# Kernel tuning notes

Hardware: AMD Instinct MI355X
Metric: run time of the kernel (lower is better)

## Reference

```python
import jax, jax.numpy as jnp
import numpy as np
from jax import lax

B, T = 4, 2048
IN_CH, SKIP_CH, OUT_CH, K = 256, 128, 128, 5
N_MAMBA, D_STATE, D_CONV, EXPAND = 2, 16, 4, 2
D_INNER = EXPAND * OUT_CH
DT_RANK = (OUT_CH + 15) // 16  # ceil(d_model/16) = 8
L = 2 * T
EPS = 1e-5


def setup_inputs() -> dict:
    key = jax.random.key(0)
    ks = jax.random.split(key, 16)
    def rn(k, shape, s=0.02):
        return jax.random.normal(k, shape, jnp.float32) * s
    A_init = jnp.broadcast_to(jnp.arange(1, D_STATE + 1, dtype=jnp.float32),
                              (N_MAMBA, 2, D_INNER, D_STATE))
    return {
        'x': rn(ks[0], (B, IN_CH, T), 1.0),
        'skip': rn(ks[1], (B, SKIP_CH, L), 1.0),
        'up_w': rn(ks[2], (IN_CH, IN_CH, K)),       # torch ConvTranspose1d weight (in,out,k)
        'up_b': jnp.zeros((IN_CH,), jnp.float32),
        'fus_w': rn(ks[3], (OUT_CH, IN_CH + SKIP_CH)),  # 1x1 conv
        'fus_b': jnp.zeros((OUT_CH,), jnp.float32),
        'gn_w': jnp.ones((OUT_CH,), jnp.float32),
        'gn_b': jnp.zeros((OUT_CH,), jnp.float32),
        'prelu_a': jnp.array(0.25, jnp.float32),
        'ln_w': jnp.ones((N_MAMBA, OUT_CH), jnp.float32),
        'ln_b': jnp.zeros((N_MAMBA, OUT_CH), jnp.float32),
        'in_w': rn(ks[4], (N_MAMBA, 2, 2 * D_INNER, OUT_CH)),
        'conv_w': rn(ks[5], (N_MAMBA, 2, D_INNER, D_CONV), 0.1),
        'conv_b': jnp.zeros((N_MAMBA, 2, D_INNER), jnp.float32),
        'xproj_w': rn(ks[6], (N_MAMBA, 2, DT_RANK + 2 * D_STATE, D_INNER)),
        'dtproj_w': rn(ks[7], (N_MAMBA, 2, D_INNER, DT_RANK), 0.1),
        'dtproj_b': rn(ks[8], (N_MAMBA, 2, D_INNER), 0.1),
        'A_log': jnp.log(A_init),
        'Dp': jnp.ones((N_MAMBA, 2, D_INNER), jnp.float32),
        'out_w': rn(ks[9], (N_MAMBA, 2, OUT_CH, D_INNER)),
    }


def _mamba_branch(xn, cw, cb, iw, xw, dw, db, Alog, Dp, ow):
    # xn: [B, L, d_model] -> [B, L, d_model]; standard Mamba selective scan.
    xz = jnp.einsum('bld,ed->ble', xn, iw)            # [B,L,2*D_INNER]
    xi, z = jnp.split(xz, 2, axis=-1)
    # causal depthwise conv over time
    xc = lax.conv_general_dilated(xi.transpose(0, 2, 1), cw[:, None, :], (1,),
                                  [(D_CONV - 1, 0)], feature_group_count=D_INNER,
                                  dimension_numbers=('NCH', 'OIH', 'NCH'))
    xi = jax.nn.silu(xc + cb[None, :, None]).transpose(0, 2, 1)  # [B,L,D_INNER]
    dbl = jnp.einsum('bld,ed->ble', xi, xw)           # [B,L,DT_RANK+2N]
    dt = jax.nn.softplus(jnp.einsum('blr,dr->bld', dbl[..., :DT_RANK], dw) + db)
    Bc = dbl[..., DT_RANK:DT_RANK + D_STATE]          # [B,L,N]
    Cc = dbl[..., DT_RANK + D_STATE:]                 # [B,L,N]
    A = -jnp.exp(Alog)                                # [D_INNER,N]
    dA = jnp.exp(dt[..., None] * A)                   # [B,L,D_INNER,N]
    dBx = dt[..., None] * Bc[:, :, None, :] * xi[..., None]
    def comb(c1, c2):
        a1, b1 = c1
        a2, b2 = c2
        return a1 * a2, a2 * b1 + b2
    _, h = lax.associative_scan(comb, (dA, dBx), axis=1)  # h_t = dA_t h_{t-1} + dBx_t
    y = jnp.einsum('bldn,bln->bld', h, Cc) + Dp * xi
    return jnp.einsum('ble,de->bld', y * jax.nn.silu(z), ow)


def _forward(x, skip, up_w, up_b, fus_w, fus_b, gn_w, gn_b, prelu_a, ln_w, ln_b,
             in_w, conv_w, conv_b, xproj_w, dtproj_w, dtproj_b, A_log, Dp, out_w):
    p = K // 2
    # ConvTranspose1d(stride=2, padding=p, output_padding=1) == lhs-dilated conv with flipped kernel
    wt = jnp.flip(up_w, -1).transpose(1, 0, 2)        # (out,in,k)
    u = lax.conv_general_dilated(x, wt, (1,), [(K - 1 - p, K - 1 - p + 1)],
                                 lhs_dilation=(2,),
                                 dimension_numbers=('NCH', 'OIH', 'NCH'))
    u = u + up_b[None, :, None]
    u = u[..., :skip.shape[-1]]
    h = jnp.concatenate([u, skip], axis=1)            # [B, in+skip, L]
    h = jnp.einsum('bct,oc->bot', h, fus_w) + fus_b[None, :, None]
    # GroupNorm(1, C): normalize over (C,T) per sample
    mu = h.mean(axis=(1, 2), keepdims=True)
    var = h.var(axis=(1, 2), keepdims=True)
    h = (h - mu) / jnp.sqrt(var + EPS) * gn_w[None, :, None] + gn_b[None, :, None]
    h = jnp.where(h >= 0, h, prelu_a * h)             # PReLU (single param)
    h = h.transpose(0, 2, 1)                          # [B, L, C]
    for i in range(N_MAMBA):
        # BiMambaBlock: pre-LN, forward + time-reversed Mamba, residual sum
        mu2 = h.mean(-1, keepdims=True)
        v2 = h.var(-1, keepdims=True)
        xn = (h - mu2) / jnp.sqrt(v2 + EPS) * ln_w[i] + ln_b[i]
        f = _mamba_branch(xn, conv_w[i, 0], conv_b[i, 0], in_w[i, 0], xproj_w[i, 0],
                          dtproj_w[i, 0], dtproj_b[i, 0], A_log[i, 0], Dp[i, 0], out_w[i, 0])
        b = _mamba_branch(jnp.flip(xn, 1), conv_w[i, 1], conv_b[i, 1], in_w[i, 1], xproj_w[i, 1],
                          dtproj_w[i, 1], dtproj_b[i, 1], A_log[i, 1], Dp[i, 1], out_w[i, 1])
        h = h + f + jnp.flip(b, 1)
    return h.transpose(0, 2, 1)                       # [B, C_out, L]


def reference(x, skip, up_w, up_b, fus_w, fus_b, gn_w, gn_b, prelu_a, ln_w, ln_b,
              in_w, conv_w, conv_b, xproj_w, dtproj_w, dtproj_b, A_log, Dp, out_w):
    return _forward(x, skip, up_w, up_b, fus_w, fus_b, gn_w, gn_b, prelu_a, ln_w, ln_b,
                    in_w, conv_w, conv_b, xproj_w, dtproj_w, dtproj_b, A_log, Dp, out_w)
```

## Files before the change

### kernel.cpp

```cpp
#include <hip/hip_runtime.h>
#include <hip/hip_bf16.h>

#define Bsz 4
#define Tt 2048
#define Ll 4096
#define NC 256
#define CH 16

typedef short bf16x8 __attribute__((ext_vector_type(8)));
typedef float f32x4 __attribute__((ext_vector_type(4)));
typedef float f32x2 __attribute__((ext_vector_type(2)));

static __device__ __forceinline__ f32x2 pk_fma(f32x2 a, f32x2 b, f32x2 c){
  f32x2 d;
  asm("v_pk_fma_f32 %0, %1, %2, %3" : "=v"(d) : "v"(a), "v"(b), "v"(c));
  return d;
}
static __device__ __forceinline__ f32x2 pk_mul(f32x2 a, f32x2 b){
  f32x2 d;
  asm("v_pk_mul_f32 %0, %1, %2" : "=v"(d) : "v"(a), "v"(b));
  return d;
}

static __device__ __forceinline__ float bs2f(unsigned short u){
  union{float f; unsigned int i;} v; v.i = ((unsigned int)u)<<16; return v.f;
}
static __device__ __forceinline__ unsigned short f2bs(float f){
  union{float f; unsigned int i;} v; v.f = f;
  unsigned int r = (v.i + 0x7fffu + ((v.i>>16)&1u)) >> 16;
  return (unsigned short)r;
}

__global__ void k_cvt(const float* __restrict__ src, unsigned short* __restrict__ dst, int n){
  int i = blockIdx.x*256 + threadIdx.x;
  if (i < n) dst[i] = f2bs(src[i]);
}

__global__ void k_prepx(const float* __restrict__ xw, unsigned short* __restrict__ wxb){
  int row = blockIdx.x, br = blockIdx.y, col = threadIdx.x;
  float v = (row < 40) ? xw[((size_t)br*40 + row)*256 + col] : 0.f;
  wxb[((size_t)br*64 + row)*256 + col] = f2bs(v);
}

__global__ void k_compose(const float* __restrict__ up_w, const float* __restrict__ fus_w,
                          const float* __restrict__ fus_b, const float* __restrict__ up_b,
                          unsigned short* __restrict__ WEb, unsigned short* __restrict__ WOb,
                          unsigned short* __restrict__ FWSb, float* __restrict__ BIAS2){
  int i = blockIdx.x;
  int o = threadIdx.x;
  float a0=0.f,a1=0.f,a2=0.f,a3=0.f,a4=0.f;
  for (int c=0;c<256;c++){
    float f = fus_w[o*384+c];
    const float* w = up_w + ((size_t)i*256+c)*5;
    a0 += f*w[0]; a1 += f*w[1]; a2 += f*w[2];
    a3 += f*w[3]; a4 += f*w[4];
  }
  WEb[(size_t)o*768 +       i] = f2bs(a4);
  WEb[(size_t)o*768 + 256 + i] = f2bs(a2);
  WEb[(size_t)o*768 + 512 + i] = f2bs(a0);
  WOb[(size_t)o*512 +       i] = f2bs(a3);
  WOb[(size_t)o*512 + 256 + i] = f2bs(a1);
  if (i<128) FWSb[o*128 + i] = f2bs(fus_w[o*384+256+i]);
  if (i==0){
    float bb = fus_b[o];
    for (int c=0;c<256;c++) bb += fus_w[o*384+c]*up_b[c];
    BIAS2[o]=bb;
  }
}

__global__ __launch_bounds__(256) void k_tx(const float* __restrict__ x, unsigned short* __restrict__ XT){
  __shared__ float tile[64][65];
  int b=blockIdx.z, t0=blockIdx.x*64, i0=blockIdx.y*64;
  int tid=threadIdx.x;
  for (int it=0;it<16;it++){
    int idx=it*256+tid; int ii=idx>>6, tt=idx&63;
    tile[ii][tt] = x[((size_t)b*256+i0+ii)*Tt + t0+tt];
  }
  __syncthreads();
  for (int it=0;it<16;it++){
    int idx=it*256+tid; int tt=idx>>6, ii=idx&63;
    XT[((size_t)b*2050 + t0+tt+1)*256 + i0+ii] = f2bs(tile[ii][tt]);
  }
}

__global__ void k_zero(unsigned short* __restrict__ XT){
  int tid=threadIdx.x;
  for (int b=0;b<Bsz;b++){
    XT[((size_t)b*2050)*256 + tid] = 0;
    XT[((size_t)b*2050+2049)*256 + tid] = 0;
  }
}

__global__ __launch_bounds__(256) void k_ts(const float* __restrict__ skip, unsigned short* __restrict__ SKT){
  __shared__ float tile[64][65];
  int b=blockIdx.z, l0=blockIdx.x*64, s0=blockIdx.y*64;
  int tid=threadIdx.x;
  for (int it=0;it<16;it++){
    int idx=it*256+tid; int ss=idx>>6, ll=idx&63;
    tile[ss][ll] = skip[((size_t)b*128+s0+ss)*Ll + l0+ll];
  }
  __syncthreads();
  for (int it=0;it<16;it++){
    int idx=it*256+tid; int ll=idx>>6, ss=idx&63;
    SKT[((size_t)b*Ll + l0+ll)*128 + s0+ss] = f2bs(tile[ss][ll]);
  }
}

__global__ __launch_bounds__(256) void k_up(const unsigned short* __restrict__ XT,
                     const unsigned short* __restrict__ SKT,
                     const unsigned short* __restrict__ WEb, const unsigned short* __restrict__ WOb,
                     const unsigned short* __restrict__ FWSb, const float* __restrict__ B2,
                     float* __restrict__ h0, float* __restrict__ gst){
  __shared__ unsigned short XL[66*264];
  __shared__ unsigned short Wb[128*72];
  __shared__ float red0[256], red1[256];
  int bt = blockIdx.x, par = blockIdx.y, b = blockIdx.z;
  int t0 = bt*64;
  int tid = threadIdx.x;
  int wave = tid>>6, lane = tid&63;
  int wm = wave>>1, wn = wave&1;
  int quad = lane>>4, l16 = lane&15;

  for (int idx=tid; idx<66*32; idx+=256){
    int row = idx>>5, c8 = idx&31;
// ... 52 lines not shown
      *(uint4*)&Wb[row*72 + c8*8] = *(const uint4*)&FWSb[(size_t)row*128 + kc*64 + c8*8];
    }
    __syncthreads();
    #pragma unroll
    for (int ks=0; ks<64; ks+=32){
      bf16x8 af[2], bf[4];
      #pragma unroll
      for (int mt=0;mt<2;mt++)
        af[mt] = *(bf16x8*)&XL[(wm*32+mt*16+l16)*136 + kc*64 + ks + quad*8];
      #pragma unroll
      for (int nt=0;nt<4;nt++)
        bf[nt] = *(bf16x8*)&Wb[(wn*64+nt*16+l16)*72 + ks + quad*8];
      #pragma unroll
      for (int mt=0;mt<2;mt++)
        #pragma unroll
        for (int nt=0;nt<4;nt++)
          acc[mt][nt] = __builtin_amdgcn_mfma_f32_16x16x32_bf16(af[mt], bf[nt], acc[mt][nt], 0,0,0);
    }
  }

  float s1=0.f, s2=0.f;
  #pragma unroll
  for (int mt=0;mt<2;mt++)
    #pragma unroll
    for (int nt=0;nt<4;nt++)
      #pragma unroll
      for (int r=0;r<4;r++){
        int m = wm*32 + mt*16 + quad*4 + r;
        int lrow = 2*(t0+m) + par;
        int col = wn*64 + nt*16 + l16;
        float v = acc[mt][nt][r] + B2[col];
        h0[((size_t)b*Ll + lrow)*128 + col] = v;
        s1 += v; s2 += v*v;
      }
  red0[tid]=s1; red1[tid]=s2;
  __syncthreads();
  for (int st=128; st>0; st>>=1){
    if (tid<st){ red0[tid]+=red0[tid+st]; red1[tid]+=red1[tid+st]; }
    __syncthreads();
  }
  if (tid==0){ atomicAdd(&gst[b*2], red0[0]); atomicAdd(&gst[b*2+1], red1[0]); }
}

__global__ void k_gnfin(float* gst){
  int b = threadIdx.x;
  if (b < Bsz){
    float n = (float)Ll*128.f;
    float mu = gst[b*2]/n;
    float var = gst[b*2+1]/n - mu*mu;
    gst[8+b]=mu; gst[12+b]=rsqrtf(var+1e-5f);
  }
}

__global__ __launch_bounds__(256) void k_gnln(const float* __restrict__ h0, const float* __restrict__ gn_w,
                      const float* __restrict__ gn_b, const float* __restrict__ pa,
                      const float* __restrict__ gst, const float* __restrict__ lnw,
                      const float* __restrict__ lnb, float* __restrict__ hres,
                      unsigned short* __restrict__ xn){
  int row = blockIdx.x*4 + (threadIdx.x>>6);
  int lane = threadIdx.x & 63;
  int b = row >> 12;
  float mu_g = gst[8+b], inv_g = gst[12+b];
  float a = pa[0];
  const float* hp = h0 + (size_t)row*128;
  float u0 = (hp[lane]   -mu_g)*inv_g*gn_w[lane]    + gn_b[lane];
  float u1 = (hp[lane+64]-mu_g)*inv_g*gn_w[lane+64] + gn_b[lane+64];
  float v0 = u0>=0.f ? u0 : a*u0;
  float v1 = u1>=0.f ? u1 : a*u1;
  float* rp = hres + (size_t)row*128;
  rp[lane] = v0; rp[lane+64] = v1;
  float s = v0+v1, q = v0*v0+v1*v1;
  #pragma unroll
  for (int off=32; off>0; off>>=1){
    s += __shfl_xor(s, off, 64);
    q += __shfl_xor(q, off, 64);
  }
  float mu = s*(1.f/128.f);
  float rs = rsqrtf(q*(1.f/128.f)-mu*mu + 1e-5f);
  unsigned short* xp = xn + (size_t)row*128;
  xp[lane]    = f2bs((v0-mu)*rs*lnw[lane]    + lnb[lane]);
  xp[lane+64] = f2bs((v1-mu)*rs*lnw[lane+64] + lnb[lane+64]);
}

__global__ __launch_bounds__(256) void k_ln(const float* __restrict__ hres, const float* __restrict__ lnw,
                     const float* __restrict__ lnb, unsigned short* __restrict__ xn){
  int row = blockIdx.x*4 + (threadIdx.x>>6);
  int lane = threadIdx.x & 63;
  const float* hp = hres + (size_t)row*128;
  float v0 = hp[lane], v1 = hp[lane+64];
  float s = v0+v1, q = v0*v0+v1*v1;
  #pragma unroll
  for (int off=32; off>0; off>>=1){
    s += __shfl_xor(s, off, 64);
    q += __shfl_xor(q, off, 64);
  }
  float mu = s*(1.f/128.f);
  float rs = rsqrtf(q*(1.f/128.f)-mu*mu + 1e-5f);
  unsigned short* xp = xn + (size_t)row*128;
  xp[lane]    = f2bs((v0-mu)*rs*lnw[lane]    + lnb[lane]);
  xp[lane+64] = f2bs((v1-mu)*rs*lnw[lane+64] + lnb[lane+64]);
}

__global__ __launch_bounds__(256) void k_gemm_in(const unsigned short* __restrict__ A,
                          const unsigned short* __restrict__ W,
                          unsigned short* __restrict__ C){
  __shared__ unsigned short As[128*72];
  __shared__ unsigned short Bs[128*72];
  int tid = threadIdx.x;
  int row0 = blockIdx.x*128;
  int n0   = blockIdx.y*128;
  int dir  = blockIdx.z;
  const unsigned short* Wp = W + (size_t)dir*512*128;
  unsigned short* Cp = C + (size_t)dir*Bsz*Ll*512;
  int wave = tid>>6, lane = tid&63;
  int wm = wave>>1, wn = wave&1;
  int quad = lane>>4, l16 = lane&15;
  f32x4 acc[4][4];
  #pragma unroll
  for (int i=0;i<4;i++)
    #pragma unroll
    for (int j=0;j<4;j++) acc[i][j] = (f32x4){0.f,0.f,0.f,0.f};

  for (int kb=0; kb<128; kb+=64){
    __syncthreads();
    #pragma unroll
    for (int it=0; it<4; it++){
      int idx = it*256 + tid;
      int row = idx>>3, c8 = idx&7;
      int r = row0 + row;
      int p = r & (Ll-1); int bb = r >> 12;
      int src = (bb<<12) + (dir ? (Ll-1-p) : p);
      *(uint4*)&As[row*72 + c8*8] = *(const uint4*)&A[(size_t)src*128 + kb + c8*8];
      *(uint4*)&Bs[row*72 + c8*8] = *(const uint4*)&Wp[(size_t)(n0+row)*128 + kb + c8*8];
    }
    __syncthreads();
    #pragma unroll
    for (int ks=0; ks<64; ks+=32){
      bf16x8 af[4], bf[4];
      #pragma unroll
      for (int mt=0;mt<4;mt++)
        af[mt] = *(bf16x8*)&As[(wm*64+mt*16+l16)*72 + ks + quad*8];
      #pragma unroll
      for (int nt=0;nt<4;nt++)
        bf[nt] = *(bf16x8*)&Bs[(wn*64+nt*16+l16)*72 + ks + quad*8];
      #pragma unroll
      for (int mt=0;mt<4;mt++)
        #pragma unroll
        for (int nt=0;nt<4;nt++)
          acc[mt][nt] = __builtin_amdgcn_mfma_f32_16x16x32_bf16(af[mt], bf[nt], acc[mt][nt], 0,0,0);
    }
  }
  #pragma unroll
  for (int mt=0;mt<4;mt++)
    #pragma unroll
    for (int nt=0;nt<4;nt++)
      #pragma unroll
      for (int r=0;r<4;r++){
        int row = row0 + wm*64 + mt*16 + quad*4 + r;
        int col = n0 + wn*64 + nt*16 + l16;
        Cp[(size_t)row*512 + col] = f2bs(acc[mt][nt][r]);
      }
}

__global__ __launch_bounds__(256) void k_gemm_out(const unsigned short* __restrict__ Y,
                           const unsigned short* __restrict__ W,
                           float* __restrict__ C){
  __shared__ unsigned short As[64*72];
  __shared__ unsigned short Bs[128*72];
  int tid = threadIdx.x;
  int row0 = blockIdx.x*64;
  int wave = tid>>6, lane = tid&63;
  int wm = wave>>1, wn = wave&1;
  int quad = lane>>4, l16 = lane&15;
  const size_t planeY = (size_t)Bsz*Ll*256;
  f32x4 acc[2][4];
  #pragma unroll
  for (int i=0;i<2;i++)
    #pragma unroll
    for (int j=0;j<4;j++) acc[i][j] = (f32x4){0.f,0.f,0.f,0.f};

  for (int kc=0; kc<8; kc++){
    int dirp = kc>>2;
    int kb = (kc&3)*64;
    const unsigned short* Wp = W + (size_t)dirp*128*256;
    __syncthreads();
    #pragma unroll
    for (int it=0; it<2; it++){
      int idx = it*256 + tid;
      int row = idx>>3, c8 = idx&7;
      int r = row0 + row;
      int p = r & (Ll-1); int bb = r >> 12;
      int srow = dirp ? ((bb<<12) + (Ll-1-p)) : r;
      *(uint4*)&As[row*72 + c8*8] = *(const uint4*)&Y[dirp*planeY + (size_t)srow*256 + kb + c8*8];
    }
    #pragma unroll
    for (int it=0; it<4; it++){
      int idx = it*256 + tid;
      int row = idx>>3, c8 = idx&7;
      *(uint4*)&Bs[row*72 + c8*8] = *(const uint4*)&Wp[(size_t)row*256 + kb + c8*8];
    }
    __syncthreads();
    #pragma unroll
    for (int ks=0; ks<64; ks+=32){
      bf16x8 af[2], bf[4];
      #pragma unroll
      for (int mt=0;mt<2;mt++)
        af[mt] = *(bf16x8*)&As[(wm*32+mt*16+l16)*72 + ks + quad*8];
      #pragma unroll
      for (int nt=0;nt<4;nt++)
        bf[nt] = *(bf16x8*)&Bs[(wn*64+nt*16+l16)*72 + ks + quad*8];
      #pragma unroll
      for (int mt=0;mt<2;mt++)
        #pragma unroll
        for (int nt=0;nt<4;nt++)
          acc[mt][nt] = __builtin_amdgcn_mfma_f32_16x16x32_bf16(af[mt], bf[nt], acc[mt][nt], 0,0,0);
    }
  }
  #pragma unroll
  for (int mt=0;mt<2;mt++)
    #pragma unroll
    for (int nt=0;nt<4;nt++)
      #pragma unroll
      for (int r=0;r<4;r++){
        int row = row0 + wm*32 + mt*16 + quad*4 + r;
        int col = wn*64 + nt*16 + l16;
        C[(size_t)row*128 + col] += acc[mt][nt][r];
      }
}

__global__ __launch_bounds__(256) void k_xproj3(const unsigned short* __restrict__ xz,
                        const unsigned short* __restrict__ wxb,
                        const float* __restrict__ cw, const float* __restrict__ cb,
                        unsigned short* __restrict__ xib, float* __restrict__ dbl){
  __shared__ unsigned short xiS[64*264];
  __shared__ unsigned short Bs[64*72];
  int tid = threadIdx.x;
  int dir = blockIdx.y;
  xz  += (size_t)dir*Bsz*Ll*512;
  wxb += (size_t)dir*64*256;
  cw  += dir*1024;
  cb  += dir*256;
  xib += (size_t)dir*Bsz*Ll*256;
  dbl += (size_t)dir*Bsz*Ll*40;
  size_t row0 = (size_t)blockIdx.x*64;
  int p0 = (int)(row0 & (Ll-1));

  {
    int d = tid;
    float4 w4 = *(const float4*)&cw[d*4];
    float bias = cb[d];
    float w0, w1, w2;
    if (p0 == 0){ w0=0.f; w1=0.f; w2=0.f; }
    else {
      w0 = bs2f(xz[(row0-3)*512 + d]);
      w1 = bs2f(xz[(row0-2)*512 + d]);
      w2 = bs2f(xz[(row0-1)*512 + d]);
    }
    #pragma unroll 4
    for (int rr=0; rr<64; rr++){
      float xv = bs2f(xz[(row0+rr)*512 + d]);
      float acc = bias + w4.x*w0 + w4.y*w1 + w4.z*w2 + w4.w*xv;
      float v = acc*__builtin_amdgcn_rcpf(1.f+__expf(-acc));
      unsigned short us = f2bs(v);
      xiS[rr*264 + d] = us;
      xib[(row0+rr)*256 + d] = us;
      w0=w1; w1=w2; w2=xv;
    }
  }

  int wave = tid>>6, lane = tid&63;
  int quad = lane>>4, l16 = lane&15;
  f32x4 acc[4];
  #pragma unroll
  for (int j=0;j<4;j++) acc[j] = (f32x4){0.f,0.f,0.f,0.f};

  for (int kb=0; kb<256; kb+=64){
    __syncthreads();
    #pragma unroll
    for (int it=0; it<2; it++){
      int idx = it*256 + tid;
      int row = idx>>3, c8 = idx&7;
      *(uint4*)&Bs[row*72 + c8*8] = *(const uint4*)&wxb[(size_t)row*256 + kb + c8*8];
    }
    __syncthreads();
    #pragma unroll
    for (int ks=0; ks<64; ks+=32){
      bf16x8 af = *(bf16x8*)&xiS[(wave*16+l16)*264 + kb + ks + quad*8];
      #pragma unroll
      for (int nt=0;nt<4;nt++){
        bf16x8 bf = *(bf16x8*)&Bs[(nt*16+l16)*72 + ks + quad*8];
        acc[nt] = __builtin_amdgcn_mfma_f32_16x16x32_bf16(af, bf, acc[nt], 0,0,0);
      }
    }
  }
  #pragma unroll
  for (int nt=0;nt<4;nt++)
    #pragma unroll
    for (int r=0;r<4;r++){
      int m = wave*16 + quad*4 + r;
      int col = nt*16 + l16;
      if (col < 40) dbl[(row0+m)*40 + col] = acc[nt][r];
    }
}

#define POWTREE2(e1, pw2) { \
  float _e2 = (e1)*(e1); \
  f32x2 _e2v = (f32x2){_e2,_e2}; \
  pw2[0] = (f32x2){(e1),_e2}; \
  pw2[1] = pk_mul(pw2[0], _e2v); \
  pw2[2] = pk_mul(pw2[1], _e2v); \
  pw2[3] = pk_mul(pw2[2], _e2v); \
  f32x2 _e8v = (f32x2){pw2[3].y, pw2[3].y}; \
  pw2[4] = pk_mul(pw2[0], _e8v); \
  pw2[5] = pk_mul(pw2[1], _e8v); \
  pw2[6] = pk_mul(pw2[2], _e8v); \
  pw2[7] = pk_mul(pw2[3], _e8v); }

__global__ __launch_bounds__(256) void k_scan1(const float* __restrict__ dbl,
                       const unsigned short* __restrict__ xib, const float* __restrict__ Alog,
                       const float* __restrict__ dtw, const float* __restrict__ dtb,
                       float* __restrict__ SD, float* __restrict__ Q){
  __shared__ float dblS[CH*24];
  int b = blockIdx.y, c = blockIdx.x, dir = blockIdx.z;
  int d = threadIdx.x;
  const float* dblP = dbl + (size_t)dir*Bsz*Ll*40;
  const unsigned short* xiP = xib + (size_t)dir*Bsz*Ll*256;
  size_t base = (size_t)b*Ll + (size_t)c*CH;
  if (d < CH*6){
    int p = d/6, j = d - p*6;
    *(float4*)&dblS[p*24 + j*4] = *(const float4*)&dblP[(base+p)*40 + j*4];
  }
  float A[16];
  #pragma unroll
  for (int j=0;j<4;j++){
    float4 a4 = *(const float4*)&Alog[(size_t)dir*4096 + d*16 + j*4];
    A[4*j]=-__expf(a4.x); A[4*j+1]=-__expf(a4.y); A[4*j+2]=-__expf(a4.z); A[4*j+3]=-__expf(a4.w);
  }
  bool chain = true;
  #pragma unroll
  for (int n=1;n<16;n++){
    float expect = A[0]*(float)(n+1);
    if (fabsf(A[n]-expect) > 1e-3f*fabsf(expect)) chain = false;
  }
  f32x2 wv2[4];
  {
    const float* dw = dtw + (size_t)dir*2048 + d*8;
    float4 w0 = *(const float4*)&dw[0];
    float4 w1 = *(const float4*)&dw[4];
    wv2[0]=(f32x2){w0.x,w0.y}; wv2[1]=(f32x2){w0.z,w0.w};
    wv2[2]=(f32x2){w1.x,w1.y}; wv2[3]=(f32x2){w1.z,w1.w};
  }
  float bbt = dtb[dir*256 + d];
  __syncthreads();
  float sdt = 0.f;
  const unsigned short* xip = xiP + base*256 + d;
  size_t sbase = (size_t)dir*Bsz*NC*4096 + ((size_t)(b*NC + c))*4096 + (size_t)d*16;
  if (chain){
    float A0 = A[0];
    bool n1 = fabsf(A0 + 1.f) < 1e-6f;
    f32x2 h2[8];
    #pragma unroll
    for (int i=0;i<8;i++) h2[i] = (f32x2){0.f,0.f};
    #pragma unroll 2
    for (int p=0;p<CH;p++){
      const float* rw = &dblS[p*24];
      f32x4 t0 = *(const f32x4*)&rw[0];
      f32x4 t1 = *(const f32x4*)&rw[4];
      f32x2 dp = pk_mul((f32x2){t0.x,t0.y}, wv2[0]);
      dp = pk_fma((f32x2){t0.z,t0.w}, wv2[1], dp);
      dp = pk_fma((f32x2){t1.x,t1.y}, wv2[2], dp);
      dp = pk_fma((f32x2){t1.z,t1.w}, wv2[3], dp);
      float a0 = bbt + dp.x + dp.y;
      float t = __expf(a0);
      float u = 1.f + t;
      float dtv = (a0>20.f)? a0 : __logf(u);
      float e1 = n1 ? __builtin_amdgcn_rcpf(u) : __expf(dtv*A0);
      float xiv = bs2f(xip[(size_t)p*256]);
      float dx = dtv*xiv;
      sdt += dtv;
      f32x2 pw2[8];
      POWTREE2(e1, pw2);
      f32x2 dxv = (f32x2){dx,dx};
      f32x4 b0 = *(const f32x4*)&rw[8];
      f32x4 b1 = *(const f32x4*)&rw[12];
      f32x4 b2 = *(const f32x4*)&rw[16];
      f32x4 b3 = *(const f32x4*)&rw[20];
      f32x2 bc2[8] = {{b0.x,b0.y},{b0.z,b0.w},{b1.x,b1.y},{b1.z,b1.w},
                      {b2.x,b2.y},{b2.z,b2.w},{b3.x,b3.y},{b3.z,b3.w}};
      #pragma unroll
      for (int i=0;i<8;i++)
        h2[i] = pk_fma(pw2[i], h2[i], pk_mul(bc2[i], dxv));
    }
    #pragma unroll
    for (int j=0;j<4;j++)
      *(float4*)&Q[sbase + 4*j] = (float4){h2[2*j].x,h2[2*j].y,h2[2*j+1].x,h2[2*j+1].y};
  } else {
    float h[16];
    #pragma unroll
    for (int n=0;n<16;n++) h[n]=0.f;
    for (int p=0;p<CH;p++){
      const float* rw = &dblS[p*24];
      float4 t0 = *(const float4*)&rw[0], t1 = *(const float4*)&rw[4];
      float a0 = bbt + t0.x*wv2[0].x+t0.y*wv2[0].y+t0.z*wv2[1].x+t0.w*wv2[1].y
                     + t1.x*wv2[2].x+t1.y*wv2[2].y+t1.z*wv2[3].x+t1.w*wv2[3].y;
      float dtv = (a0>20.f)? a0 : __logf(1.f+__expf(a0));
      float xiv = bs2f(xip[(size_t)p*256]);
      float dx = dtv*xiv;
      sdt += dtv;
      float bc[16];
      *(float4*)&bc[0]  = *(const float4*)&rw[8];
      *(float4*)&bc[4]  = *(const float4*)&rw[12];
      *(float4*)&bc[8]  = *(const float4*)&rw[16];
      *(float4*)&bc[12] = *(const float4*)&rw[20];
      #pragma unroll
      for (int n=0;n<16;n++){
        float a = __expf(dtv*A[n]);
        h[n] = a*h[n] + bc[n]*dx;
      }
    }
    #pragma unroll
    for (int j=0;j<4;j++)
      *(float4*)&Q[sbase + 4*j] = (float4){h[4*j],h[4*j+1],h[4*j+2],h[4*j+3]};
  }
  SD[(((size_t)dir*Bsz + b)*NC + c)*256 + d] = sdt;
}

__global__ __launch_bounds__(64) void k_scan2(const float* __restrict__ SD, float* __restrict__ Q,
                                              const float* __restrict__ Alog){
  int b = blockIdx.y, dir = blockIdx.z;
  int t = blockIdx.x*64 + threadIdx.x;
  int dn4 = t*4;
  int d = dn4 >> 4;
  float4 A4;
  {
    const float* ap = Alog + (size_t)dir*4096 + dn4;
    A4.x = -__expf(ap[0]); A4.y = -__expf(ap[1]);
    A4.z = -__expf(ap[2]); A4.w = -__expf(ap[3]);
  }
  const float* sd = SD + (((size_t)dir*Bsz + b)*NC)*256 + d;
  float* q = Q + (size_t)dir*Bsz*NC*4096 + (size_t)b*NC*4096 + dn4;
  float4 H = {0.f,0.f,0.f,0.f};
  float  s_n = sd[0];
  float4 q_n = *(const float4*)q;
  for (int c=0;c<NC;c++){
    float s_c = s_n; float4 q_c = q_n;
    if (c+1 < NC){
      s_n = sd[(size_t)(c+1)*256];
      q_n = *(const float4*)(q + (size_t)(c+1)*4096);
    }
    float4 p;
    p.x = __expf(A4.x*s_c); p.y = __expf(A4.y*s_c);
    p.z = __expf(A4.z*s_c); p.w = __expf(A4.w*s_c);
    *(float4*)(q + (size_t)c*4096) = H;
    H.x = p.x*H.x + q_c.x; H.y = p.y*H.y + q_c.y;
    H.z = p.z*H.z + q_c.z; H.w = p.w*H.w + q_c.w;
  }
}

__global__ __launch_bounds__(256) void k_scan3(const float* __restrict__ dbl,
                       unsigned short* xiy, const float* __restrict__ Alog,
                       const float* __restrict__ dtw, const float* __restrict__ dtb,
                       const float* __restrict__ Dpw, const float* __restrict__ Hs,
                       const unsigned short* __restrict__ xz){
  __shared__ float dblS[CH*40];
  int b = blockIdx.y, c = blockIdx.x, dir = blockIdx.z;
  int d = threadIdx.x;
  const float* dblP = dbl + (size_t)dir*Bsz*Ll*40;
  unsigned short* xiP = xiy + (size_t)dir*Bsz*Ll*256;
  const unsigned short* xzP = xz + (size_t)dir*Bsz*Ll*512;
  size_t base = (size_t)b*Ll + (size_t)c*CH;
  for (int idx=d; idx<CH*10; idx+=256){
    int p = idx/10, j = idx - p*10;
    *(float4*)&dblS[p*40 + j*4] = *(const float4*)&dblP[(base+p)*40 + j*4];
  }
  float A[16];
  #pragma unroll
  for (int j=0;j<4;j++){
    float4 a4 = *(const float4*)&Alog[(size_t)dir*4096 + d*16 + j*4];
    A[4*j]=-__expf(a4.x); A[4*j+1]=-__expf(a4.y); A[4*j+2]=-__expf(a4.z); A[4*j+3]=-__expf(a4.w);
  }
  bool chain = true;
  #pragma unroll
  for (int n=1;n<16;n++){
    float expect = A[0]*(float)(n+1);
    if (fabsf(A[n]-expect) > 1e-3f*fabsf(expect)) chain = false;
  }
  f32x2 wv2[4];
  {
    const float* dw = dtw + (size_t)dir*2048 + d*8;
    float4 w0 = *(const float4*)&dw[0];
    float4 w1 = *(const float4*)&dw[4];
    wv2[0]=(f32x2){w0.x,w0.y}; wv2[1]=(f32x2){w0.z,w0.w};
    wv2[2]=(f32x2){w1.x,w1.y}; wv2[3]=(f32x2){w1.z,w1.w};
  }
  float bbt = dtb[dir*256 + d];
  float Dp = Dpw[dir*256 + d];
  size_t sbase = (size_t)dir*Bsz*NC*4096 + ((size_t)(b*NC + c))*4096 + (size_t)d*16;
  __syncthreads();
  unsigned short* xip = xiP + base*256 + d;
  const unsigned short* zp = xzP + base*512 + 256 + d;
  if (chain){
    float A0 = A[0];
    bool n1 = fabsf(A0 + 1.f) < 1e-6f;
    f32x2 h2[8];
    #pragma unroll
    for (int j=0;j<4;j++){
      float4 h4 = *(const float4*)&Hs[sbase + 4*j];
      h2[2*j]   = (f32x2){h4.x,h4.y};
      h2[2*j+1] = (f32x2){h4.z,h4.w};
    }
    #pragma unroll 2
    for (int p=0;p<CH;p++){
      const float* rw = &dblS[p*40];
      f32x4 t0 = *(const f32x4*)&rw[0];
      f32x4 t1 = *(const f32x4*)&rw[4];
      f32x2 dp = pk_mul((f32x2){t0.x,t0.y}, wv2[0]);
      dp = pk_fma((f32x2){t0.z,t0.w}, wv2[1], dp);
      dp = pk_fma((f32x2){t1.x,t1.y}, wv2[2], dp);
      dp = pk_fma((f32x2){t1.z,t1.w}, wv2[3], dp);
      float a0 = bbt + dp.x + dp.y;
      float t = __expf(a0);
      float u = 1.f + t;
      float dtv = (a0>20.f)? a0 : __logf(u);
      float e1 = n1 ? __builtin_amdgcn_rcpf(u) : __expf(dtv*A0);
      float xiv = bs2f(xip[(size_t)p*256]);
      float dx = dtv*xiv;
      f32x2 pw2[8];
      POWTREE2(e1, pw2);
      f32x2 dxv = (f32x2){dx,dx};
      f32x4 b0 = *(const f32x4*)&rw[8];
      f32x4 b1 = *(const f32x4*)&rw[12];
      f32x4 b2 = *(const f32x4*)&rw[16];
      f32x4 b3 = *(const f32x4*)&rw[20];
      f32x4 c0 = *(const f32x4*)&rw[24];
      f32x4 c1 = *(const f32x4*)&rw[28];
      f32x4 c2 = *(const f32x4*)&rw[32];
      f32x4 c3 = *(const f32x4*)&rw[36];
      f32x2 bc2[8] = {{b0.x,b0.y},{b0.z,b0.w},{b1.x,b1.y},{b1.z,b1.w},
                      {b2.x,b2.y},{b2.z,b2.w},{b3.x,b3.y},{b3.z,b3.w}};
      f32x2 cc2[8] = {{c0.x,c0.y},{c0.z,c0.w},{c1.x,c1.y},{c1.z,c1.w},
                      {c2.x,c2.y},{c2.z,c2.w},{c3.x,c3.y},{c3.z,c3.w}};
      f32x2 ya;
      h2[0] = pk_fma(pw2[0], h2[0], pk_mul(bc2[0], dxv));
      ya = pk_mul(h2[0], cc2[0]);
      #pragma unroll
      for (int i=1;i<8;i++){
        h2[i] = pk_fma(pw2[i], h2[i], pk_mul(bc2[i], dxv));
        ya = pk_fma(h2[i], cc2[i], ya);
      }
      float acc = ya.x + ya.y;
      float z = bs2f(zp[(size_t)p*512]);
      float g = z*__builtin_amdgcn_rcpf(1.f+__expf(-z));
      xip[(size_t)p*256] = f2bs((acc + Dp*xiv)*g);
    }
  } else {
    float h[16];
    #pragma unroll
    for (int j=0;j<4;j++){
      float4 h4 = *(const float4*)&Hs[sbase + 4*j];
      h[4*j]=h4.x; h[4*j+1]=h4.y; h[4*j+2]=h4.z; h[4*j+3]=h4.w;
    }
    for (int p=0;p<CH;p++){
      const float* rw = &dblS[p*40];
      float4 t0 = *(const float4*)&rw[0], t1 = *(const float4*)&rw[4];
      float a0 = bbt + t0.x*wv2[0].x+t0.y*wv2[0].y+t0.z*wv2[1].x+t0.w*wv2[1].y
                     + t1.x*wv2[2].x+t1.y*wv2[2].y+t1.z*wv2[3].x+t1.w*wv2[3].y;
      float dtv = (a0>20.f)? a0 : __logf(1.f+__expf(a0));
      float xiv = bs2f(xip[(size_t)p*256]);
      float dx = dtv*xiv;
      float bc[16], cc[16];
      *(float4*)&bc[0]  = *(const float4*)&rw[8];
      *(float4*)&bc[4]  = *(const float4*)&rw[12];
      *(float4*)&bc[8]  = *(const float4*)&rw[16];
      *(float4*)&bc[12] = *(const float4*)&rw[20];
      *(float4*)&cc[0]  = *(const float4*)&rw[24];
      *(float4*)&cc[4]  = *(const float4*)&rw[28];
      *(float4*)&cc[8]  = *(const float4*)&rw[32];
      *(float4*)&cc[12] = *(const float4*)&rw[36];
      float acc = 0.f;
      #pragma unroll
      for (int n=0;n<16;n++){
        float a = __expf(dtv*A[n]);
        h[n] = a*h[n] + bc[n]*dx;
        acc += h[n]*cc[n];
      }
      float z = bs2f(zp[(size_t)p*512]);
      float g = z*__builtin_amdgcn_rcpf(1.f+__expf(-z));
      xip[(size_t)p*256] = f2bs((acc + Dp*xiv)*g);
    }
  }
}

__global__ __launch_bounds__(256) void k_final(const float* __restrict__ hres, float* __restrict__ out){
  __shared__ float tile[64*129];
  int b = blockIdx.y, l0 = blockIdx.x*64;
  int tid = threadIdx.x;
  for (int q=0;q<32;q++){
    int idx = q*256 + tid;
    int l = idx >> 7, c = idx & 127;
    tile[l*129 + c] = hres[((size_t)b*Ll + l0 + l)*128 + c];
  }
  __syncthreads();
  int lo = tid & 63; int cbase = tid >> 6;
  for (int q=0;q<32;q++){
    int c = cbase + q*4;
    out[((size_t)b*128 + c)*Ll + l0 + lo] = tile[lo*129 + c];
  }
}

extern "C" void kernel_launch(void* const* d_in, const int* in_sizes, int n_in,
                              void* d_out, int out_size, void* d_ws, size_t ws_size,
                              hipStream_t stream){
  const float* x      = (const float*)d_in[0];
  const float* skip   = (const float*)d_in[1];
  const float* up_w   = (const float*)d_in[2];
  const float* up_b   = (const float*)d_in[3];
  const float* fus_w  = (const float*)d_in[4];
  const float* fus_b  = (const float*)d_in[5];
  const float* gn_w   = (const float*)d_in[6];
  const float* gn_b   = (const float*)d_in[7];
  const float* pa     = (const float*)d_in[8];
  const float* ln_w   = (const float*)d_in[9];
  const float* ln_b   = (const float*)d_in[10];
  const float* in_w   = (const float*)d_in[11];
  const float* conv_w = (const float*)d_in[12];
  const float* conv_b = (const float*)d_in[13];
  const float* xproj_w= (const float*)d_in[14];
  const float* dtproj_w=(const float*)d_in[15];
  const float* dtproj_b=(const float*)d_in[16];
  const float* A_log  = (const float*)d_in[17];
  const float* Dp     = (const float*)d_in[18];
  const float* out_w  = (const float*)d_in[19];

  float* w = (float*)d_ws;
  size_t off=0;
  float* B2 = w+off; off += 128;
  float* GST= w+off; off += 16;
  off = (off+3)&~(size_t)3;
  float* HR = w+off; off += (size_t)Bsz*Ll*128;
  float* DBL2= w+off; off += 2*(size_t)Bsz*Ll*40;
  unsigned short* XNB = (unsigned short*)(w+off); off += (size_t)Bsz*Ll*128/2;
  unsigned short* XZB2= (unsigned short*)(w+off); off += 2*(size_t)Bsz*Ll*512/2;
  unsigned short* IWB = (unsigned short*)(w+off); off += 2*2*512*128/2;
  unsigned short* OWB = (unsigned short*)(w+off); off += 2*2*128*256/2;
  unsigned short* WXB = (unsigned short*)(w+off); off += 2*2*64*256/2;
  unsigned short* WEb = (unsigned short*)(w+off); off += 768*128/2;
  unsigned short* WOb = (unsigned short*)(w+off); off += 512*128/2;
  unsigned short* FWSb= (unsigned short*)(w+off); off += 128*128/2;
  size_t planeS = (size_t)Bsz*NC*4096;
  float* U1 = w+off; off += 2*planeS;
  unsigned short* XT  = (unsigned short*)U1;
  unsigned short* SKT = (unsigned short*)(U1 + 1049604);
  float* SQ = U1;
  float* SD = (float*)XNB;
  float* U2 = w+off; off += 2*(size_t)Bsz*Ll*128;
  float* H0 = U2;
  unsigned short* XIB2 = (unsigned short*)U2;

  hipMemsetAsync(GST, 0, 16*sizeof(float), stream);
  k_cvt<<<(2*2*512*128+255)/256,256,0,stream>>>(in_w, IWB, 2*2*512*128);
  k_cvt<<<(2*2*128*256+255)/256,256,0,stream>>>(out_w, OWB, 2*2*128*256);
  k_prepx<<<dim3(64,4),256,0,stream>>>(xproj_w, WXB);
  k_compose<<<256,128,0,stream>>>(up_w, fus_w, fus_b, up_b, WEb, WOb, FWSb, B2);
  k_tx<<<dim3(Tt/64, 4, Bsz),256,0,stream>>>(x, XT);
  k_zero<<<1,256,0,stream>>>(XT);
  k_ts<<<dim3(Ll/64, 2, Bsz),256,0,stream>>>(skip, SKT);
  k_up<<<dim3(32, 2, Bsz),256,0,stream>>>(XT, SKT, WEb, WOb, FWSb, B2, H0, GST);
  k_gnfin<<<1,64,0,stream>>>(GST);
  k_gnln<<<Bsz*Ll/4,256,0,stream>>>(H0, gn_w, gn_b, pa, GST, ln_w, ln_b, HR, XNB);
  for (int i=0;i<2;i++){
    if (i==1) k_ln<<<Bsz*Ll/4,256,0,stream>>>(HR, ln_w + 128, ln_b + 128, XNB);
    k_gemm_in<<<dim3(128,4,2),256,0,stream>>>(XNB, IWB + (size_t)(i*2)*512*128, XZB2);
    k_xproj3<<<dim3(Bsz*Ll/64,2),256,0,stream>>>(XZB2, WXB + (size_t)(i*2)*64*256,
                                                 conv_w + (i*2)*1024, conv_b + (i*2)*256,
                                                 XIB2, DBL2);
    k_scan1<<<dim3(NC,Bsz,2),256,0,stream>>>(DBL2, XIB2, A_log + (i*2)*4096,
                                             dtproj_w + (i*2)*2048, dtproj_b + (i*2)*256, SD, SQ);
    k_scan2<<<dim3(16,Bsz,2),64,0,stream>>>(SD, SQ, A_log + (i*2)*4096);
    k_scan3<<<dim3(NC,Bsz,2),256,0,stream>>>(DBL2, XIB2, A_log + (i*2)*4096,
                                             dtproj_w + (i*2)*2048, dtproj_b + (i*2)*256,
                                             Dp + (i*2)*256, SQ, XZB2);
    k_gemm_out<<<256,256,0,stream>>>(XIB2, OWB + (size_t)(i*2)*128*256, HR);
  }
  k_final<<<dim3(Ll/64,Bsz),256,0,stream>>>(HR, (float*)d_out);
}
```

Baseline: 422.8 us.

## Fuse second LayerNorm into out-GEMM, precompute A tables, preload scan inputs

Removes the standalone LayerNorm kernel between Mamba layers by computing row mean/variance inside the first out-projection GEMM epilogue with a shared-memory reduction. A new prep kernel precomputes -exp(A_log), A0 and the chain flag once instead of in every scan block. The scan kernels now preload the x and z values for a chunk into registers and fully unroll the time loop. This trades more registers and a block-wide sync for fewer kernel launches, less repeated exp work and fewer global round trips.

Result: faster. 412.4 us (-2.5%).

```diff
diff --git a/kernel.cpp b/kernel.cpp
--- a/kernel.cpp
+++ b/kernel.cpp
@@ -21,6 +21,8 @@
   asm("v_pk_mul_f32 %0, %1, %2" : "=v"(d) : "v"(a), "v"(b));
   return d;
 }
+static __device__ __forceinline__ f32x2 lo2(f32x4 v){ return (f32x2){v.x, v.y}; }
+static __device__ __forceinline__ f32x2 hi2(f32x4 v){ return (f32x2){v.z, v.w}; }
 
 static __device__ __forceinline__ float bs2f(unsigned short u){
   union{float f; unsigned int i;} v; v.i = ((unsigned int)u)<<16; return v.f;
@@ -40,6 +42,27 @@
   int row = blockIdx.x, br = blockIdx.y, col = threadIdx.x;
   float v = (row < 40) ? xw[((size_t)br*40 + row)*256 + col] : 0.f;
   wxb[((size_t)br*64 + row)*256 + col] = f2bs(v);
+}
+
+__global__ void k_prepA(const float* __restrict__ Alog, float* __restrict__ AEX,
+                        float* __restrict__ A0C, float* __restrict__ CHN){
+  int br = blockIdx.x, d = threadIdx.x;
+  float A[16];
+  #pragma unroll
+  for (int j=0;j<4;j++){
+    float4 a4 = *(const float4*)&Alog[(size_t)br*4096 + d*16 + j*4];
+    A[4*j]  = -__expf(a4.x); A[4*j+1] = -__expf(a4.y);
+    A[4*j+2]= -__expf(a4.z); A[4*j+3] = -__expf(a4.w);
+    *(float4*)&AEX[(size_t)br*4096 + d*16 + j*4] = (float4){A[4*j],A[4*j+1],A[4*j+2],A[4*j+3]};
+  }
+  bool chain = true;
+  #pragma unroll
+  for (int n=1;n<16;n++){
+    float expect = A[0]*(float)(n+1);
+    if (fabsf(A[n]-expect) > 1e-3f*fabsf(expect)) chain = false;
+  }
+  A0C[br*256 + d] = A[0];
+  CHN[br*256 + d] = chain ? 1.f : 0.f;
 }
 
 __global__ void k_compose(const float* __restrict__ up_w, const float* __restrict__ fus_w,
@@ -258,25 +281,6 @@
   xp[lane+64] = f2bs((v1-mu)*rs*lnw[lane+64] + lnb[lane+64]);
 }
 
-__global__ __launch_bounds__(256) void k_ln(const float* __restrict__ hres, const float* __restrict__ lnw,
-                     const float* __restrict__ lnb, unsigned short* __restrict__ xn){
-  int row = blockIdx.x*4 + (threadIdx.x>>6);
-  int lane = threadIdx.x & 63;
-  const float* hp = hres + (size_t)row*128;
-  float v0 = hp[lane], v1 = hp[lane+64];
-  float s = v0+v1, q = v0*v0+v1*v1;
-  #pragma unroll
-  for (int off=32; off>0; off>>=1){
-    s += __shfl_xor(s, off, 64);
-    q += __shfl_xor(q, off, 64);
-  }
-  float mu = s*(1.f/128.f);
-  float rs = rsqrtf(q*(1.f/128.f)-mu*mu + 1e-5f);
-  unsigned short* xp = xn + (size_t)row*128;
-  xp[lane]    = f2bs((v0-mu)*rs*lnw[lane]    + lnb[lane]);
-  xp[lane+64] = f2bs((v1-mu)*rs*lnw[lane+64] + lnb[lane+64]);
-}
-
 __global__ __launch_bounds__(256) void k_gemm_in(const unsigned short* __restrict__ A,
                           const unsigned short* __restrict__ W,
                           unsigned short* __restrict__ C){
@@ -338,11 +342,14 @@
       }
 }
 
-__global__ __launch_bounds__(256) void k_gemm_out(const unsigned short* __restrict__ Y,
+template<int DO_LN>
+__global__ __launch_bounds__(256) void k_gemm_out_t(const unsigned short* __restrict__ Y,
                            const unsigned short* __restrict__ W,
-                           float* __restrict__ C){
+                           float* __restrict__ C, const float* __restrict__ lnw,
+                           const float* __restrict__ lnb, unsigned short* __restrict__ xn){
   __shared__ unsigned short As[64*72];
   __shared__ unsigned short Bs[128*72];
+  __shared__ float redS[2][4][2][4][2][2];
   int tid = threadIdx.x;
   int row0 = blockIdx.x*64;
   int wave = tid>>6, lane = tid&63;
@@ -392,6 +399,8 @@
           acc[mt][nt] = __builtin_amdgcn_mfma_f32_16x16x32_bf16(af[mt], bf[nt], acc[mt][nt], 0,0,0);
     }
   }
+
+  float vals[2][4][4];
   #pragma unroll
   for (int mt=0;mt<2;mt++)
     #pragma unroll
@@ -400,8 +409,46 @@
       for (int r=0;r<4;r++){
         int row = row0 + wm*32 + mt*16 + quad*4 + r;
         int col = wn*64 + nt*16 + l16;
-        C[(size_t)row*128 + col] += acc[mt][nt][r];
+        float v = C[(size_t)row*128 + col] + acc[mt][nt][r];
+        C[(size_t)row*128 + col] = v;
+        vals[mt][nt][r] = v;
       }
+
+  if (DO_LN){
+    #pragma unroll
+    for (int mt=0;mt<2;mt++)
+      #pragma unroll
+      for (int r=0;r<4;r++){
+        float s = 0.f, q = 0.f;
+        #pragma unroll
+        for (int nt=0;nt<4;nt++){ float v = vals[mt][nt][r]; s += v; q += v*v; }
+        #pragma unroll
+        for (int off=1; off<16; off<<=1){
+          s += __shfl_xor(s, off, 64);
+          q += __shfl_xor(q, off, 64);
+        }
+        if (l16 == 0){
+          redS[wm][quad][mt][r][wn][0] = s;
+          redS[wm][quad][mt][r][wn][1] = q;
+        }
+      }
+    __syncthreads();
+    #pragma unroll
+    for (int mt=0;mt<2;mt++)
+      #pragma unroll
+      for (int r=0;r<4;r++){
+        float s = redS[wm][quad][mt][r][0][0] + redS[wm][quad][mt][r][1][0];
+        float q = redS[wm][quad][mt][r][0][1] + redS[wm][quad][mt][r][1][1];
+        float mu = s*(1.f/128.f);
+        float rs = rsqrtf(q*(1.f/128.f) - mu*mu + 1e-5f);
+        int row = row0 + wm*32 + mt*16 + quad*4 + r;
+        #pragma unroll
+        for (int nt=0;nt<4;nt++){
+          int col = wn*64 + nt*16 + l16;
+          xn[(size_t)row*128 + col] = f2bs((vals[mt][nt][r]-mu)*rs*lnw[col] + lnb[col]);
+        }
+      }
+  }
 }
 
 __global__ __launch_bounds__(256) void k_xproj3(const unsigned short* __restrict__ xz,
@@ -493,7 +540,8 @@
   pw2[7] = pk_mul(pw2[3], _e8v); }
 
 __global__ __launch_bounds__(256) void k_scan1(const float* __restrict__ dbl,
-                       const unsigned short* __restrict__ xib, const float* __restrict__ Alog,
+                       const unsigned short* __restrict__ xib, const float* __restrict__ AEX,
+                       const float* __restrict__ A0C, const float* __restrict__ CHNf,
                        const float* __restrict__ dtw, const float* __restrict__ dtb,
                        float* __restrict__ SD, float* __restrict__ Q){
   __shared__ float dblS[CH*24];
@@ -506,18 +554,8 @@
     int p = d/6, j = d - p*6;
     *(float4*)&dblS[p*24 + j*4] = *(const float4*)&dblP[(base+p)*40 + j*4];
   }
-  float A[16];
-  #pragma unroll
-  for (int j=0;j<4;j++){
-    float4 a4 = *(const float4*)&Alog[(size_t)dir*4096 + d*16 + j*4];
-    A[4*j]=-__expf(a4.x); A[4*j+1]=-__expf(a4.y); A[4*j+2]=-__expf(a4.z); A[4*j+3]=-__expf(a4.w);
-  }
-  bool chain = true;
-  #pragma unroll
-  for (int n=1;n<16;n++){
-    float expect = A[0]*(float)(n+1);
-    if (fabsf(A[n]-expect) > 1e-3f*fabsf(expect)) chain = false;
-  }
+  float A0 = A0C[dir*256 + d];
+  bool chain = CHNf[dir*256 + d] != 0.f;
   f32x2 wv2[4];
   {
     const float* dw = dtw + (size_t)dir*2048 + d*8;
@@ -532,45 +570,53 @@
   const unsigned short* xip = xiP + base*256 + d;
   size_t sbase = (size_t)dir*Bsz*NC*4096 + ((size_t)(b*NC + c))*4096 + (size_t)d*16;
   if (chain){
-    float A0 = A[0];
     bool n1 = fabsf(A0 + 1.f) < 1e-6f;
+    float xv[CH];
+    #pragma unroll
+    for (int p=0;p<CH;p++) xv[p] = bs2f(xip[(size_t)p*256]);
     f32x2 h2[8];
     #pragma unroll
     for (int i=0;i<8;i++) h2[i] = (f32x2){0.f,0.f};
-    #pragma unroll 2
+    #pragma unroll
     for (int p=0;p<CH;p++){
       const float* rw = &dblS[p*24];
       f32x4 t0 = *(const f32x4*)&rw[0];
       f32x4 t1 = *(const f32x4*)&rw[4];
-      f32x2 dp = pk_mul((f32x2){t0.x,t0.y}, wv2[0]);
-      dp = pk_fma((f32x2){t0.z,t0.w}, wv2[1], dp);
-      dp = pk_fma((f32x2){t1.x,t1.y}, wv2[2], dp);
-      dp = pk_fma((f32x2){t1.z,t1.w}, wv2[3], dp);
+      f32x2 dp = pk_mul(lo2(t0), wv2[0]);
+      dp = pk_fma(hi2(t0), wv2[1], dp);
+      dp = pk_fma(lo2(t1), wv2[2], dp);
+      dp = pk_fma(hi2(t1), wv2[3], dp);
       float a0 = bbt + dp.x + dp.y;
       float t = __expf(a0);
       float u = 1.f + t;
       float dtv = (a0>20.f)? a0 : __logf(u);
       float e1 = n1 ? __builtin_amdgcn_rcpf(u) : __expf(dtv*A0);
-      float xiv = bs2f(xip[(size_t)p*256]);
-      float dx = dtv*xiv;
+      float dx = dtv*xv[p];
       sdt += dtv;
       f32x2 pw2[8];
       POWTREE2(e1, pw2);
       f32x2 dxv = (f32x2){dx,dx};
-      f32x4 b0 = *(const f32x4*)&rw[8];
-      f32x4 b1 = *(const f32x4*)&rw[12];
-      f32x4 b2 = *(const f32x4*)&rw[16];
-      f32x4 b3 = *(const f32x4*)&rw[20];
-      f32x2 bc2[8] = {{b0.x,b0.y},{b0.z,b0.w},{b1.x,b1.y},{b1.z,b1.w},
-                      {b2.x,b2.y},{b2.z,b2.w},{b3.x,b3.y},{b3.z,b3.w}};
-      #pragma unroll
-      for (int i=0;i<8;i++)
-        h2[i] = pk_fma(pw2[i], h2[i], pk_mul(bc2[i], dxv));
+      f32x4 b0 = *(const f32x4*)&dblS[p*24+8];
+      f32x4 b1 = *(const f32x4*)&dblS[p*24+12];
+      f32x4 b2 = *(const f32x4*)&dblS[p*24+16];
+      f32x4 b3 = *(const f32x4*)&dblS[p*24+20];
+      h2[0] = pk_fma(pw2[0], h2[0], pk_mul(lo2(b0), dxv));
+      h2[1] = pk_fma(pw2[1], h2[1], pk_mul(hi2(b0), dxv));
+      h2[2] = pk_fma(pw2[2], h2[2], pk_mul(lo2(b1), dxv));
+      h2[3] = pk_fma(pw2[3], h2[3], pk_mul(hi2(b1), dxv));
+      h2[4] = pk_fma(pw2[4], h2[4], pk_mul(lo2(b2), dxv));
+      h2[5] = pk_fma(pw2[5], h2[5], pk_mul(hi2(b2), dxv));
+      h2[6] = pk_fma(pw2[6], h2[6], pk_mul(lo2(b3), dxv));
+      h2[7] = pk_fma(pw2[7], h2[7], pk_mul(hi2(b3), dxv));
     }
     #pragma unroll
     for (int j=0;j<4;j++)
       *(float4*)&Q[sbase + 4*j] = (float4){h2[2*j].x,h2[2*j].y,h2[2*j+1].x,h2[2*j+1].y};
   } else {
+    float A[16];
+    #pragma unroll
+    for (int j=0;j<4;j++)
+      *(float4*)&A[4*j] = *(const float4*)&AEX[(size_t)dir*4096 + d*16 + j*4];
     float h[16];
     #pragma unroll
     for (int n=0;n<16;n++) h[n]=0.f;
@@ -602,17 +648,12 @@
 }
 
 __global__ __launch_bounds__(64) void k_scan2(const float* __restrict__ SD, float* __restrict__ Q,
-                                              const float* __restrict__ Alog){
+                                              const float* __restrict__ AEX){
   int b = blockIdx.y, dir = blockIdx.z;
   int t = blockIdx.x*64 + threadIdx.x;
   int dn4 = t*4;
   int d = dn4 >> 4;
-  float4 A4;
-  {
-    const float* ap = Alog + (size_t)dir*4096 + dn4;
-    A4.x = -__expf(ap[0]); A4.y = -__expf(ap[1]);
-    A4.z = -__expf(ap[2]); A4.w = -__expf(ap[3]);
-  }
+  float4 A4 = *(const float4*)&AEX[(size_t)dir*4096 + dn4];
   const float* sd = SD + (((size_t)dir*Bsz + b)*NC)*256 + d;
   float* q = Q + (size_t)dir*Bsz*NC*4096 + (size_t)b*NC*4096 + dn4;
   float4 H = {0.f,0.f,0.f,0.f};
@@ -634,7 +675,8 @@
 }
 
 __global__ __launch_bounds__(256) void k_scan3(const float* __restrict__ dbl,
-                       unsigned short* xiy, const float* __restrict__ Alog,
+                       unsigned short* xiy, const float* __restrict__ AEX,
+                       const float* __restrict__ A0C, const float* __restrict__ CHNf,
                        const float* __restrict__ dtw, const float* __restrict__ dtb,
                        const float* __restrict__ Dpw, const float* __restrict__ Hs,
                        const unsigned short* __restrict__ xz){
@@ -649,18 +691,8 @@
     int p = idx/10, j = idx - p*10;
     *(float4*)&dblS[p*40 + j*4] = *(const float4*)&dblP[(base+p)*40 + j*4];
   }
-  float A[16];
-  #pragma unroll
-  for (int j=0;j<4;j++){
-    float4 a4 = *(const float4*)&Alog[(size_t)dir*4096 + d*16 + j*4];
-    A[4*j]=-__expf(a4.x); A[4*j+1]=-__expf(a4.y); A[4*j+2]=-__expf(a4.z); A[4*j+3]=-__expf(a4.w);
-  }
-  bool chain = true;
-  #pragma unroll
-  for (int n=1;n<16;n++){
-    float expect = A[0]*(float)(n+1);
-    if (fabsf(A[n]-expect) > 1e-3f*fabsf(expect)) chain = false;
-  }
+  float A0 = A0C[dir*256 + d];
+  bool chain = CHNf[dir*256 + d] != 0.f;
   f32x2 wv2[4];
   {
     const float* dw = dtw + (size_t)dir*2048 + d*8;
@@ -676,8 +708,12 @@
   unsigned short* xip = xiP + base*256 + d;
   const unsigned short* zp = xzP + base*512 + 256 + d;
   if (chain){
-    float A0 = A[0];
     bool n1 = fabsf(A0 + 1.f) < 1e-6f;
+    float xv[CH], zv[CH];
+    #pragma unroll
+    for (int p=0;p<CH;p++) xv[p] = bs2f(xip[(size_t)p*256]);
+    #pragma unroll
+    for (int p=0;p<CH;p++) zv[p] = bs2f(zp[(size_t)p*512]);
     f32x2 h2[8];
     #pragma unroll
     for (int j=0;j<4;j++){
@@ -685,51 +721,59 @@
       h2[2*j]   = (f32x2){h4.x,h4.y};
       h2[2*j+1] = (f32x2){h4.z,h4.w};
     }
-    #pragma unroll 2
+    #pragma unroll
     for (int p=0;p<CH;p++){
       const float* rw = &dblS[p*40];
       f32x4 t0 = *(const f32x4*)&rw[0];
       f32x4 t1 = *(const f32x4*)&rw[4];
-      f32x2 dp = pk_mul((f32x2){t0.x,t0.y}, wv2[0]);
-      dp = pk_fma((f32x2){t0.z,t0.w}, wv2[1], dp);
-      dp = pk_fma((f32x2){t1.x,t1.y}, wv2[2], dp);
-      dp = pk_fma((f32x2){t1.z,t1.w}, wv2[3], dp);
+      f32x2 dp = pk_mul(lo2(t0), wv2[0]);
+      dp = pk_fma(hi2(t0), wv2[1], dp);
+      dp = pk_fma(lo2(t1), wv2[2], dp);
+      dp = pk_fma(hi2(t1), wv2[3], dp);
       float a0 = bbt + dp.x + dp.y;
       float t = __expf(a0);
       float u = 1.f + t;
       float dtv = (a0>20.f)? a0 : __logf(u);
       float e1 = n1 ? __builtin_amdgcn_rcpf(u) : __expf(dtv*A0);
-      float xiv = bs2f(xip[(size_t)p*256]);
-      float dx = dtv*xiv;
+      float dx = dtv*xv[p];
       f32x2 pw2[8];
       POWTREE2(e1, pw2);
       f32x2 dxv = (f32x2){dx,dx};
-      f32x4 b0 = *(const f32x4*)&rw[8];
-      f32x4 b1 = *(const f32x4*)&rw[12];
-      f32x4 b2 = *(const f32x4*)&rw[16];
-      f32x4 b3 = *(const f32x4*)&rw[20];
-      f32x4 c0 = *(const f32x4*)&rw[24];
-      f32x4 c1 = *(const f32x4*)&rw[28];
-      f32x4 c2 = *(const f32x4*)&rw[32];
-      f32x4 c3 = *(const f32x4*)&rw[36];
-      f32x2 bc2[8] = {{b0.x,b0.y},{b0.z,b0.w},{b1.x,b1.y},{b1.z,b1.w},
-                      {b2.x,b2.y},{b2.z,b2.w},{b3.x,b3.y},{b3.z,b3.w}};
-      f32x2 cc2[8] = {{c0.x,c0.y},{c0.z,c0.w},{c1.x,c1.y},{c1.z,c1.w},
-                      {c2.x,c2.y},{c2.z,c2.w},{c3.x,c3.y},{c3.z,c3.w}};
+      f32x4 b0 = *(const f32x4*)&dblS[p*40+8];
+      f32x4 b1 = *(const f32x4*)&dblS[p*40+12];
+      f32x4 b2 = *(const f32x4*)&dblS[p*40+16];
+      f32x4 b3 = *(const f32x4*)&dblS[p*40+20];
+      f32x4 c0 = *(const f32x4*)&dblS[p*40+24];
+      f32x4 c1 = *(const f32x4*)&dblS[p*40+28];
+      f32x4 c2 = *(const f32x4*)&dblS[p*40+32];
+      f32x4 c3 = *(const f32x4*)&dblS[p*40+36];
       f32x2 ya;
-      h2[0] = pk_fma(pw2[0], h2[0], pk_mul(bc2[0], dxv));
-      ya = pk_mul(h2[0], cc2[0]);
-      #pragma unroll
-      for (int i=1;i<8;i++){
-        h2[i] = pk_fma(pw2[i], h2[i], pk_mul(bc2[i], dxv));
-        ya = pk_fma(h2[i], cc2[i], ya);
-      }
+      h2[0] = pk_fma(pw2[0], h2[0], pk_mul(lo2(b0), dxv));
+      ya = pk_mul(h2[0], lo2(c0));
+      h2[1] = pk_fma(pw2[1], h2[1], pk_mul(hi2(b0), dxv));
+      ya = pk_fma(h2[1], hi2(c0), ya);
+      h2[2] = pk_fma(pw2[2], h2[2], pk_mul(lo2(b1), dxv));
+      ya = pk_fma(h2[2], lo2(c1), ya);
+      h2[3] = pk_fma(pw2[3], h2[3], pk_mul(hi2(b1), dxv));
+      ya = pk_fma(h2[3], hi2(c1), ya);
+      h2[4] = pk_fma(pw2[4], h2[4], pk_mul(lo2(b2), dxv));
+      ya = pk_fma(h2[4], lo2(c2), ya);
+      h2[5] = pk_fma(pw2[5], h2[5], pk_mul(hi2(b2), dxv));
+      ya = pk_fma(h2[5], hi2(c2), ya);
+      h2[6] = pk_fma(pw2[6], h2[6], pk_mul(lo2(b3), dxv));
+      ya = pk_fma(h2[6], lo2(c3), ya);
+      h2[7] = pk_fma(pw2[7], h2[7], pk_mul(hi2(b3), dxv));
+      ya = pk_fma(h2[7], hi2(c3), ya);
       float acc = ya.x + ya.y;
-      float z = bs2f(zp[(size_t)p*512]);
+      float z = zv[p];
       float g = z*__builtin_amdgcn_rcpf(1.f+__expf(-z));
-      xip[(size_t)p*256] = f2bs((acc + Dp*xiv)*g);
+      xip[(size_t)p*256] = f2bs((acc + Dp*xv[p])*g);
     }
   } else {
+    float A[16];
+    #pragma unroll
+    for (int j=0;j<4;j++)
+      *(float4*)&A[4*j] = *(const float4*)&AEX[(size_t)dir*4096 + d*16 + j*4];
     float h[16];
     #pragma unroll
     for (int j=0;j<4;j++){
@@ -823,6 +867,9 @@
   unsigned short* WEb = (unsigned short*)(w+off); off += 768*128/2;
   unsigned short* WOb = (unsigned short*)(w+off); off += 512*128/2;
   unsigned short* FWSb= (unsigned short*)(w+off); off += 128*128/2;
+  float* AEXb = w+off; off += 4*4096;
+  float* A0Cb = w+off; off += 4*256;
+  float* CHNb = w+off; off += 4*256;
   size_t planeS = (size_t)Bsz*NC*4096;
   float* U1 = w+off; off += 2*planeS;
   unsigned short* XT  = (unsigned short*)U1;
@@ -837,6 +884,7 @@
   k_cvt<<<(2*2*512*128+255)/256,256,0,stream>>>(in_w, IWB, 2*2*512*128);
   k_cvt<<<(2*2*128*256+255)/256,256,0,stream>>>(out_w, OWB, 2*2*128*256);
   k_prepx<<<dim3(64,4),256,0,stream>>>(xproj_w, WXB);
+  k_prepA<<<4,256,0,stream>>>(A_log, AEXb, A0Cb, CHNb);
   k_compose<<<256,128,0,stream>>>(up_w, fus_w, fus_b, up_b, WEb, WOb, FWSb, B2);
   k_tx<<<dim3(Tt/64, 4, Bsz),256,0,stream>>>(x, XT);
   k_zero<<<1,256,0,stream>>>(XT);
@@ -845,18 +893,24 @@
   k_gnfin<<<1,64,0,stream>>>(GST);
   k_gnln<<<Bsz*Ll/4,256,0,stream>>>(H0, gn_w, gn_b, pa, GST, ln_w, ln_b, HR, XNB);
   for (int i=0;i<2;i++){
-    if (i==1) k_ln<<<Bsz*Ll/4,256,0,stream>>>(HR, ln_w + 128, ln_b + 128, XNB);
     k_gemm_in<<<dim3(128,4,2),256,0,stream>>>(XNB, IWB + (size_t)(i*2)*512*128, XZB2);
     k_xproj3<<<dim3(Bsz*Ll/64,2),256,0,stream>>>(XZB2, WXB + (size_t)(i*2)*64*256,
                                                  conv_w + (i*2)*1024, conv_b + (i*2)*256,
                                                  XIB2, DBL2);
-    k_scan1<<<dim3(NC,Bsz,2),256,0,stream>>>(DBL2, XIB2, A_log + (i*2)*4096,
+    k_scan1<<<dim3(NC,Bsz,2),256,0,stream>>>(DBL2, XIB2, AEXb + (size_t)(i*2)*4096,
+                                             A0Cb + (i*2)*256, CHNb + (i*2)*256,
                                              dtproj_w + (i*2)*2048, dtproj_b + (i*2)*256, SD, SQ);
-    k_scan2<<<dim3(16,Bsz,2),64,0,stream>>>(SD, SQ, A_log + (i*2)*4096);
-    k_scan3<<<dim3(NC,Bsz,2),256,0,stream>>>(DBL2, XIB2, A_log + (i*2)*4096,
+    k_scan2<<<dim3(16,Bsz,2),64,0,stream>>>(SD, SQ, AEXb + (size_t)(i*2)*4096);
+    k_scan3<<<dim3(NC,Bsz,2),256,0,stream>>>(DBL2, XIB2, AEXb + (size_t)(i*2)*4096,
+                                             A0Cb + (i*2)*256, CHNb + (i*2)*256,
                                              dtproj_w + (i*2)*2048, dtproj_b + (i*2)*256,
                                              Dp + (i*2)*256, SQ, XZB2);
-    k_gemm_out<<<256,256,0,stream>>>(XIB2, OWB + (size_t)(i*2)*128*256, HR);
+    if (i==0)
+      k_gemm_out_t<1><<<256,256,0,stream>>>(XIB2, OWB + 0, HR, ln_w + 128, ln_b + 128, XNB);
+    else
+      k_gemm_out_t<0><<<256,256,0,stream>>>(XIB2, OWB + (size_t)2*128*256, HR,
+                                            (const float*)nullptr, (const float*)nullptr,
+                                            (unsigned short*)nullptr);
   }
   k_final<<<dim3(Ll/64,Bsz),256,0,stream>>>(HR, (float*)d_out);
 }
```
